# Kernel optimization log

Hardware: AMD Instinct MI355X
Metric: run time of the kernel (lower is better)

The kernel has to match this reference:

```python
import jax, jax.numpy as jnp
import numpy as np

B, C, Q, E = 32, 1024, 128, 512

def setup_inputs() -> dict:
    key = jax.random.key(0)
    k1, k2, k3 = jax.random.split(key, 3)
    context = jax.random.normal(k1, (B, C, E), dtype=jnp.float32)
    question = jax.random.normal(k2, (B, Q, E), dtype=jnp.float32)
    # ws = [ws_q | ws_c | ws_m], matching cat([q, ctx, q*ctx]) order
    ws = jax.random.normal(k3, (3 * E,), dtype=jnp.float32) * (1.0 / np.sqrt(E))
    return {"context": context, "question": question, "ws": ws}

def reference(context, question, ws):
    ws_q, ws_c, ws_m = ws[:E], ws[E:2 * E], ws[2 * E:]
    # similarity[b,c,q] = ws_q.q[b,q] + ws_c.c[b,c] + ws_m.(q[b,q]*c[b,c])
    sim = (jnp.einsum('bqe,e->bq', question, ws_q)[:, None, :]
           + jnp.einsum('bce,e->bc', context, ws_c)[:, :, None]
           + jnp.einsum('bce,bqe,e->bcq', context, question, ws_m))  # (B,C,Q)
    c2q = jnp.einsum('bcq,bqe->bce', jax.nn.softmax(sim, axis=2), question)  # (B,C,E)
    q2c_w = jax.nn.softmax(jnp.max(sim, axis=2), axis=1)  # (B,C)
    q2c = jnp.einsum('bc,bce->be', q2c_w, context)[:, None, :]  # (B,1,E)
    return (c2q, q2c)
```

## Files before the change

kernel.cpp:

```cpp
#include <hip/hip_runtime.h>

#define BB 32
#define CC 1024
#define QQ 128
#define EE 512

typedef unsigned int uint32;
typedef unsigned short u16;
typedef __bf16 bf16x8 __attribute__((ext_vector_type(8)));
typedef float f32x4 __attribute__((ext_vector_type(4)));

#define QMF_OFF  (0u)
#define QTF_OFF  (4u<<20)
#define PV_OFF   (8u<<20)
#define QD_OFF   (12u<<20)
#define MT_OFF   ((12u<<20) + 16384u)
#define ST_OFF   (MT_OFF + 8192u)

__device__ __forceinline__ u16 bfc(float f){
  __bf16 h = (__bf16)f;
  return __builtin_bit_cast(u16, h);
}

__global__ __launch_bounds__(256) void k_prep_qm(const float* __restrict__ q,
                                                 const float* __restrict__ ws,
                                                 unsigned char* __restrict__ wsp){
  const int b = blockIdx.x >> 2, et = blockIdx.x & 3, e0 = et*128;
  __shared__ u16 tile[128*136];
  const int tid = threadIdx.x;
  #pragma unroll
  for (int i=0;i<16;i++){
    int id = tid + i*256;
    int qi = id >> 5;
    int el = (id & 31) << 2;
    float4 v = *(const float4*)(q + (size_t)(b*QQ+qi)*EE + e0 + el);
    float4 m = *(const float4*)(ws + 2*EE + e0 + el);
    float4 c = *(const float4*)(ws +   EE + e0 + el);
    ushort4 u; u.x = bfc(v.x*m.x + c.x); u.y = bfc(v.y*m.y + c.y);
               u.z = bfc(v.z*m.z + c.z); u.w = bfc(v.w*m.w + c.w);
    *(ushort4*)&tile[qi*136 + el] = u;
  }
  __syncthreads();
  const int lane = tid & 63, wv = tid >> 6, l15 = lane & 15, l4 = lane >> 4;
  uint4* qmf = (uint4*)(wsp + QMF_OFF);
  #pragma unroll
  for (int i=0;i<8;i++){
    int f = wv*8 + i;
    int kl = f >> 3, nf = f & 7;
    uint4 u = *(const uint4*)&tile[(nf*16 + l15)*136 + kl*32 + l4*8];
    qmf[(size_t)((b*16 + et*4 + kl)*8 + nf)*64 + lane] = u;
  }
}

__global__ __launch_bounds__(256) void k_prep_qt(const float* __restrict__ q,
                                                 unsigned char* __restrict__ wsp){
  const int b = blockIdx.x >> 2, et = blockIdx.x & 3, e0 = et*128;
  __shared__ u16 tile[128*136];
  const int tid = threadIdx.x;
  #pragma unroll
  for (int i=0;i<16;i++){
    int id = tid + i*256;
    int qi = id >> 5;
    int el = (id & 31) << 2;
    float4 v = *(const float4*)(q + (size_t)(b*QQ+qi)*EE + e0 + el);
    ushort4 u; u.x = bfc(v.x); u.y = bfc(v.y); u.z = bfc(v.z); u.w = bfc(v.w);
    *(ushort4*)&tile[qi*136 + el] = u;
  }
  __syncthreads();
  const int lane = tid & 63, wv = tid >> 6, l15 = lane & 15, l4 = lane >> 4;
  uint4* qtf = (uint4*)(wsp + QTF_OFF);
  #pragma unroll
  for (int i=0;i<8;i++){
    int f = wv*8 + i;
    int ks2 = f >> 3, nl = f & 7, ne = et*8 + nl;
    uint32 x[4];
    #pragma unroll
    for (int p=0;p<4;p++){
      u16 t0 = tile[(ks2*32 + l4*8 + 2*p    )*136 + nl*16 + l15];
      u16 t1 = tile[(ks2*32 + l4*8 + 2*p + 1)*136 + nl*16 + l15];
      x[p] = (uint32)t0 | ((uint32)t1 << 16);
    }
    uint4 u; u.x = x[0]; u.y = x[1]; u.z = x[2]; u.w = x[3];
    qtf[(size_t)((b*4 + ks2)*32 + ne)*64 + lane] = u;
  }
}

__global__ __launch_bounds__(256) void k_prep_qd(const float* __restrict__ q,
                                                 const float* __restrict__ ws,
                                                 unsigned char* __restrict__ wsp){
  const int row = blockIdx.x*4 + (threadIdx.x >> 6);
  const int lane = threadIdx.x & 63;
  const float4* qr = (const float4*)(q + (size_t)row*EE) + lane*2;
  const float4* wq = (const float4*)ws + lane*2;
  float4 v0 = qr[0], v1 = qr[1], a0 = wq[0], a1 = wq[1];
  float dot = v0.x*a0.x + v0.y*a0.y + v0.z*a0.z + v0.w*a0.w
            + v1.x*a1.x + v1.y*a1.y + v1.z*a1.z + v1.w*a1.w;
  #pragma unroll
  for (int off=1; off<64; off<<=1) dot += __shfl_xor(dot, off);
  if (lane == 0) ((float*)(wsp + QD_OFF))[row] = dot;
}

__global__ __launch_bounds__(256, 4) void k_main(const float* __restrict__ ctx,
                                                 unsigned char* __restrict__ wsp,
                                                 float* __restrict__ out){
  __shared__ __align__(16) unsigned char Ast[2][8192];
  __shared__ float smax_s[2][2][16];
  __shared__ float ssum_s[2][2][16];
  __shared__ float wrow_s[2][2][16];

  const int bid = blockIdx.x;
  const int sw  = (bid & 7)*128 + (bid >> 3);
  const int b   = sw >> 5;
  const int t   = sw & 31;
  const int tid = threadIdx.x;
  const int lane = tid & 63;
  const int w    = tid >> 6;
  const int rg   = w >> 1;
  const int h    = w & 1;
  const int l15  = lane & 15;
  const int l4   = lane >> 4;
  const int r0   = t*32 + rg*16;

  const float* qdp = (const float*)(wsp + QD_OFF) + b*QQ + h*64 + l15;
  float qd[4];
  #pragma unroll
  for (int n=0;n<4;n++) qd[n] = qdp[n*16];

  const unsigned char* cbase = (const unsigned char*)(ctx + (size_t)(b*CC + t*32)*EE);
  int srcoff[2];
  #pragma unroll
  for (int j=0;j<2;j++){
    int row = j*16 + w*4 + (lane>>4);
    int gp  = (lane & 15) ^ (row & 7);
    srcoff[j] = row*2048 + gp*16;
  }
  auto stage = [&](int c){
    unsigned char* bufb = Ast[c & 1];
    #pragma unroll
    for (int j=0;j<2;j++){
      const unsigned char* g = cbase + srcoff[j] + c*256;
      __builtin_amdgcn_global_load_lds(
        (const __attribute__((address_space(1))) uint32*)g,
        (__attribute__((address_space(3))) uint32*)(bufb + j*4096 + w*1024),
        16, 0, 0);
    }
  };

  f32x4 acc[4];
  #pragma unroll
  for (int n=0;n<4;n++) acc[n] = (f32x4){0.f,0.f,0.f,0.f};
  const int arow = rg*16 + l15;
  const int a7   = arow & 7;
  const uint4* qmf = (const uint4*)(wsp + QMF_OFF) + (size_t)b*8192 + h*256 + lane;

  stage(0);
  __syncthreads();
  #pragma unroll
  for (int c=0; c<8; c++){
    if (c < 7) stage(c+1);
    const unsigned char* ab = Ast[c&1] + arow*256;
    #pragma unroll
    for (int s=0; s<2; s++){
      uint4 f0 = *(const uint4*)(ab + ((s*8 + ((l4*2+0) ^ a7))*16));
      uint4 f1 = *(const uint4*)(ab + ((s*8 + ((l4*2+1) ^ a7))*16));
      const float* p0 = (const float*)&f0;
      const float* p1 = (const float*)&f1;
      bf16x8 af;
      af[0]=(__bf16)p0[0]; af[1]=(__bf16)p0[1]; af[2]=(__bf16)p0[2]; af[3]=(__bf16)p0[3];
      af[4]=(__bf16)p1[0]; af[5]=(__bf16)p1[1]; af[6]=(__bf16)p1[2]; af[7]=(__bf16)p1[3];
      #pragma unroll
      for (int n=0;n<4;n++){
        bf16x8 bq = __builtin_bit_cast(bf16x8, qmf[((c*2+s)*8 + n)*64]);
        acc[n] = __builtin_amdgcn_mfma_f32_16x16x32_bf16(af, bq, acc[n], 0, 0, 0);
      }
    }
    __syncthreads();
  }

  float mxh[4];
  #pragma unroll
  for (int r=0;r<4;r++){
    float m = -3.0e38f;
    #pragma unroll
    for (int n=0;n<4;n++){
      float v = acc[n][r] + qd[n];
      acc[n][r] = v;
      m = fmaxf(m, v);
    }
    m = fmaxf(m, __shfl_xor(m,1));
    m = fmaxf(m, __shfl_xor(m,2));
    m = fmaxf(m, __shfl_xor(m,4));
    m = fmaxf(m, __shfl_xor(m,8));
    mxh[r] = m;
  }
  if (l15 == 0){
    #pragma unroll
    for (int r=0;r<4;r++) smax_s[rg][h][l4*4 + r] = mxh[r];
  }
  __syncthreads();
  float mx[4];
  #pragma unroll
  for (int r=0;r<4;r++) mx[r] = fmaxf(smax_s[rg][0][l4*4+r], smax_s[rg][1][l4*4+r]);

  u16* pfr = (u16*)Ast[0];
  const int l4p = l15 >> 3;
  const int jj  = l15 & 7;
  #pragma unroll
  for (int r=0;r<4;r++){
    float s = 0.f;
    #pragma unroll
    for (int n=0;n<4;n++){
      float p = __expf(acc[n][r] - mx[r]);
      __bf16 hb = (__bf16)p;
      s += (float)hb;
      pfr[(rg*4 + (h<<1) + (n>>1))*512 + ((((n&1)<<1)|l4p)*16 + l4*4 + r)*8 + jj] = __builtin_bit_cast(u16, hb);
    }
    s += __shfl_xor(s,1); s += __shfl_xor(s,2); s += __shfl_xor(s,4); s += __shfl_xor(s,8);
    if (l15 == 0) ssum_s[rg][h][l4*4 + r] = s;
  }

  float m16 = fmaxf(fmaxf(mx[0],mx[1]), fmaxf(mx[2],mx[3]));
  m16 = fmaxf(m16, __shfl_xor(m16,16));
  m16 = fmaxf(m16, __shfl_xor(m16,32));
  float wr[4], s16 = 0.f;
  #pragma unroll
  for (int r=0;r<4;r++){ wr[r] = __expf(mx[r] - m16); s16 += wr[r]; }
  s16 += __shfl_xor(s16,16);
  s16 += __shfl_xor(s16,32);
  if (l15 == 0){
    #pragma unroll
    for (int r=0;r<4;r++) wrow_s[rg][h][l4*4 + r] = wr[r];
  }
  if (h == 0 && lane == 0){
    ((float*)(wsp + MT_OFF))[b*64 + t*2 + rg] = m16;
    ((float*)(wsp + ST_OFF))[b*64 + t*2 + rg] = s16;
  }
  __syncthreads();
  float rden[4];
  #pragma unroll
  for (int r=0;r<4;r++) rden[r] = 1.f/(ssum_s[rg][0][l4*4+r] + ssum_s[rg][1][l4*4+r]);

  const uint4* qt4 = (const uint4*)(wsp + QTF_OFF) + (size_t)b*8192 + lane;
  const uint4* pf  = (const uint4*)(Ast[0] + rg*4096);
  float* ob = out + (size_t)(b*CC + r0)*EE + h*256;
  #pragma unroll
  for (int pp=0; pp<2; pp++){
    f32x4 acc2[8];
    #pragma unroll
    for (int n2=0;n2<8;n2++) acc2[n2] = (f32x4){0.f,0.f,0.f,0.f};
    #pragma unroll
    for (int ks2=0; ks2<4; ks2++){
      bf16x8 a = __builtin_bit_cast(bf16x8, pf[ks2*64 + lane]);
      #pragma unroll
      for (int n2=0;n2<8;n2++){
        const int ne = h*16 + pp*8 + n2;
        bf16x8 bq = __builtin_bit_cast(bf16x8, qt4[(ks2*32 + ne)*64]);
        acc2[n2] = __builtin_amdgcn_mfma_f32_16x16x32_bf16(a, bq, acc2[n2], 0, 0, 0);
      }
    }
    #pragma unroll
    for (int n2=0;n2<8;n2++){
      #pragma unroll
      for (int r=0;r<4;r++)
        ob[(size_t)(l4*4 + r)*EE + pp*128 + n2*16 + l15] = acc2[n2][r]*rden[r];
    }
  }

  {
    const float4* cb = (const float4*)(ctx + (size_t)(b*CC + r0)*EE + h*256) + lane;
    float4 a4; a4.x = 0.f; a4.y = 0.f; a4.z = 0.f; a4.w = 0.f;
    #pragma unroll
    for (int rr=0; rr<16; rr++){
      float wv = wrow_s[rg][h][rr];
      float4 g = cb[(size_t)rr*128];
      a4.x = fmaf(wv, g.x, a4.x); a4.y = fmaf(wv, g.y, a4.y);
      a4.z = fmaf(wv, g.z, a4.z); a4.w = fmaf(wv, g.w, a4.w);
    }
    float* pv = (float*)(wsp + PV_OFF) + (size_t)(b*64 + t*2 + rg)*EE + h*256 + lane*4;
    *(float4*)pv = a4;
  }
}

__global__ __launch_bounds__(256) void k_fin(unsigned char* __restrict__ wsp,
                                             float* __restrict__ out){
  const int b = blockIdx.x;
  __shared__ float sc_s[64];
  const int tid = threadIdx.x;
  if (tid < 64){
    float Mg = ((const float*)(wsp + MT_OFF))[b*64 + tid];
    float Sg = ((const float*)(wsp + ST_OFF))[b*64 + tid];
    float M = Mg;
    #pragma unroll
    for (int off=1; off<64; off<<=1) M = fmaxf(M, __shfl_xor(M, off));
    float ev = __expf(Mg - M);
    float ds = ev * Sg;
    #pragma unroll
    for (int off=1; off<64; off<<=1) ds += __shfl_xor(ds, off);
    sc_s[tid] = ev / ds;
  }
  __syncthreads();
  const float* pv = (const float*)(wsp + PV_OFF) + (size_t)b*64*EE;
  float a0 = 0.f, a1 = 0.f;
  #pragma unroll 8
  for (int g=0; g<64; g++){
    float s = sc_s[g];
    a0 = fmaf(s, pv[g*EE + tid],       a0);
    a1 = fmaf(s, pv[g*EE + tid + 256], a1);
  }
  size_t base = (size_t)BB*CC*EE + (size_t)b*EE;
  out[base + tid]       = a0;
  out[base + tid + 256] = a1;
}

extern "C" void kernel_launch(void* const* d_in, const int* in_sizes, int n_in,
                              void* d_out, int out_size, void* d_ws, size_t ws_size,
                              hipStream_t stream){
  const float* ctx = (const float*)d_in[0];
  const float* q   = (const float*)d_in[1];
  const float* ws  = (const float*)d_in[2];
  float* out = (float*)d_out;
  unsigned char* wsp = (unsigned char*)d_ws;

  k_prep_qm<<<dim3(BB*4),    dim3(256), 0, stream>>>(q, ws, wsp);
  k_prep_qt<<<dim3(BB*4),    dim3(256), 0, stream>>>(q, wsp);
  k_prep_qd<<<dim3(BB*QQ/4), dim3(256), 0, stream>>>(q, ws, wsp);
  k_main   <<<dim3(1024),    dim3(256), 0, stream>>>(ctx, wsp, out);
  k_fin    <<<dim3(BB),      dim3(256), 0, stream>>>(wsp, out);
}
```

Baseline: 62.64 us.

## Load full context tile to registers, convert to bf16 once, prefetch MFMA operands

Replaces the double-buffered global_load_lds staging of fp32 context chunks with a single bulk register load of the whole 32x512 tile. The tile is converted to bf16 once and stored into a swizzled 32KB LDS buffer, so the per-chunk __syncthreads and the per-MFMA fp32-to-bf16 conversion go away. Both GEMM loops now software-pipeline their B-operand loads one or two steps ahead and preload the P fragments into registers. The cost is more LDS (32KB instead of 16KB) and many more live registers, which may lower occupancy under the 4-blocks launch bound and removes the overlap between context loading and compute.

```diff
diff --git a/kernel.cpp b/kernel.cpp
--- a/kernel.cpp
+++ b/kernel.cpp
@@ -103,7 +103,7 @@
 __global__ __launch_bounds__(256, 4) void k_main(const float* __restrict__ ctx,
                                                  unsigned char* __restrict__ wsp,
                                                  float* __restrict__ out){
-  __shared__ __align__(16) unsigned char Ast[2][8192];
+  __shared__ __align__(16) unsigned char Ast[32*1024];
   __shared__ float smax_s[2][2][16];
   __shared__ float ssum_s[2][2][16];
   __shared__ float wrow_s[2][2][16];
@@ -126,55 +126,61 @@
   #pragma unroll
   for (int n=0;n<4;n++) qd[n] = qdp[n*16];
 
-  const unsigned char* cbase = (const unsigned char*)(ctx + (size_t)(b*CC + t*32)*EE);
-  int srcoff[2];
-  #pragma unroll
-  for (int j=0;j<2;j++){
-    int row = j*16 + w*4 + (lane>>4);
-    int gp  = (lane & 15) ^ (row & 7);
-    srcoff[j] = row*2048 + gp*16;
-  }
-  auto stage = [&](int c){
-    unsigned char* bufb = Ast[c & 1];
-    #pragma unroll
-    for (int j=0;j<2;j++){
-      const unsigned char* g = cbase + srcoff[j] + c*256;
-      __builtin_amdgcn_global_load_lds(
-        (const __attribute__((address_space(1))) uint32*)g,
-        (__attribute__((address_space(3))) uint32*)(bufb + j*4096 + w*1024),
-        16, 0, 0);
-    }
-  };
+  const int srow = w*8 + (lane >> 3);
+  const int scol = (lane & 7)*64;
+  const float4* src = (const float4*)(ctx + (size_t)(b*CC + t*32 + srow)*EE + scol);
+  float4 v[16];
+  #pragma unroll
+  for (int j=0;j<16;j++) v[j] = src[j];
+
+  {
+    unsigned char* drow = Ast + srow*1024;
+    const int dswz = (srow & 7) << 4;
+    #pragma unroll
+    for (int i=0;i<8;i++){
+      float4 x = v[2*i], y = v[2*i+1];
+      uint4 u;
+      u.x = (uint32)bfc(x.x) | ((uint32)bfc(x.y) << 16);
+      u.y = (uint32)bfc(x.z) | ((uint32)bfc(x.w) << 16);
+      u.z = (uint32)bfc(y.x) | ((uint32)bfc(y.y) << 16);
+      u.w = (uint32)bfc(y.z) | ((uint32)bfc(y.w) << 16);
+      *(uint4*)(drow + ((((lane & 7)*128) + i*16) ^ dswz)) = u;
+    }
+  }
+  __syncthreads();
+
+  const int arow = rg*16 + l15;
+  const unsigned char* ap = Ast + arow*1024;
+  const int a7 = (arow & 7) << 4;
+  const uint4* qmf = (const uint4*)(wsp + QMF_OFF) + (size_t)b*8192 + h*256 + lane;
 
   f32x4 acc[4];
   #pragma unroll
   for (int n=0;n<4;n++) acc[n] = (f32x4){0.f,0.f,0.f,0.f};
-  const int arow = rg*16 + l15;
-  const int a7   = arow & 7;
-  const uint4* qmf = (const uint4*)(wsp + QMF_OFF) + (size_t)b*8192 + h*256 + lane;
-
-  stage(0);
-  __syncthreads();
-  #pragma unroll
-  for (int c=0; c<8; c++){
-    if (c < 7) stage(c+1);
-    const unsigned char* ab = Ast[c&1] + arow*256;
-    #pragma unroll
-    for (int s=0; s<2; s++){
-      uint4 f0 = *(const uint4*)(ab + ((s*8 + ((l4*2+0) ^ a7))*16));
-      uint4 f1 = *(const uint4*)(ab + ((s*8 + ((l4*2+1) ^ a7))*16));
-      const float* p0 = (const float*)&f0;
-      const float* p1 = (const float*)&f1;
-      bf16x8 af;
-      af[0]=(__bf16)p0[0]; af[1]=(__bf16)p0[1]; af[2]=(__bf16)p0[2]; af[3]=(__bf16)p0[3];
-      af[4]=(__bf16)p1[0]; af[5]=(__bf16)p1[1]; af[6]=(__bf16)p1[2]; af[7]=(__bf16)p1[3];
+
+  bf16x8 afc = __builtin_bit_cast(bf16x8, *(const uint4*)(ap + ((0*64 + l4*16) ^ a7)));
+  uint4 bq0[4], bq1[4];
+  #pragma unroll
+  for (int n=0;n<4;n++) bq0[n] = qmf[(0*8 + n)*64];
+  #pragma unroll
+  for (int n=0;n<4;n++) bq1[n] = qmf[(1*8 + n)*64];
+
+  #pragma unroll
+  for (int ks=0; ks<16; ks++){
+    bf16x8 afn;
+    if (ks < 15)
+      afn = __builtin_bit_cast(bf16x8, *(const uint4*)(ap + (((ks+1)*64 + l4*16) ^ a7)));
+    uint4 bqn[4];
+    if (ks < 14){
       #pragma unroll
-      for (int n=0;n<4;n++){
-        bf16x8 bq = __builtin_bit_cast(bf16x8, qmf[((c*2+s)*8 + n)*64]);
-        acc[n] = __builtin_amdgcn_mfma_f32_16x16x32_bf16(af, bq, acc[n], 0, 0, 0);
-      }
-    }
-    __syncthreads();
+      for (int n=0;n<4;n++) bqn[n] = qmf[((ks+2)*8 + n)*64];
+    }
+    #pragma unroll
+    for (int n=0;n<4;n++)
+      acc[n] = __builtin_amdgcn_mfma_f32_16x16x32_bf16(afc, __builtin_bit_cast(bf16x8, bq0[n]), acc[n], 0, 0, 0);
+    afc = afn;
+    #pragma unroll
+    for (int n=0;n<4;n++){ bq0[n] = bq1[n]; bq1[n] = bqn[n]; }
   }
 
   float mxh[4];
@@ -183,9 +189,9 @@
     float m = -3.0e38f;
     #pragma unroll
     for (int n=0;n<4;n++){
-      float v = acc[n][r] + qd[n];
-      acc[n][r] = v;
-      m = fmaxf(m, v);
+      float vv = acc[n][r] + qd[n];
+      acc[n][r] = vv;
+      m = fmaxf(m, vv);
     }
     m = fmaxf(m, __shfl_xor(m,1));
     m = fmaxf(m, __shfl_xor(m,2));
@@ -202,7 +208,7 @@
   #pragma unroll
   for (int r=0;r<4;r++) mx[r] = fmaxf(smax_s[rg][0][l4*4+r], smax_s[rg][1][l4*4+r]);
 
-  u16* pfr = (u16*)Ast[0];
+  u16* pfr = (u16*)Ast;
   const int l4p = l15 >> 3;
   const int jj  = l15 & 7;
   #pragma unroll
@@ -241,22 +247,35 @@
   for (int r=0;r<4;r++) rden[r] = 1.f/(ssum_s[rg][0][l4*4+r] + ssum_s[rg][1][l4*4+r]);
 
   const uint4* qt4 = (const uint4*)(wsp + QTF_OFF) + (size_t)b*8192 + lane;
-  const uint4* pf  = (const uint4*)(Ast[0] + rg*4096);
+  const uint4* pf  = (const uint4*)(Ast + rg*4096);
+  bf16x8 pa[4];
+  #pragma unroll
+  for (int ks2=0; ks2<4; ks2++) pa[ks2] = __builtin_bit_cast(bf16x8, pf[ks2*64 + lane]);
   float* ob = out + (size_t)(b*CC + r0)*EE + h*256;
+
   #pragma unroll
   for (int pp=0; pp<2; pp++){
+    const int ne0 = h*16 + pp*8;
     f32x4 acc2[8];
     #pragma unroll
     for (int n2=0;n2<8;n2++) acc2[n2] = (f32x4){0.f,0.f,0.f,0.f};
-    #pragma unroll
-    for (int ks2=0; ks2<4; ks2++){
-      bf16x8 a = __builtin_bit_cast(bf16x8, pf[ks2*64 + lane]);
+    uint4 bqc[4];
+    #pragma unroll
+    for (int n=0;n<4;n++) bqc[n] = qt4[(0*32 + ne0 + n)*64];
+    #pragma unroll
+    for (int u=0; u<8; u++){
+      const int ks2 = u >> 1, hf = u & 1;
+      uint4 bqn[4];
+      if (u < 7){
+        const int u2 = u + 1;
+        #pragma unroll
+        for (int n=0;n<4;n++) bqn[n] = qt4[((u2>>1)*32 + ne0 + (u2&1)*4 + n)*64];
+      }
       #pragma unroll
-      for (int n2=0;n2<8;n2++){
-        const int ne = h*16 + pp*8 + n2;
-        bf16x8 bq = __builtin_bit_cast(bf16x8, qt4[(ks2*32 + ne)*64]);
-        acc2[n2] = __builtin_amdgcn_mfma_f32_16x16x32_bf16(a, bq, acc2[n2], 0, 0, 0);
-      }
+      for (int n=0;n<4;n++)
+        acc2[hf*4+n] = __builtin_amdgcn_mfma_f32_16x16x32_bf16(pa[ks2], __builtin_bit_cast(bf16x8, bqc[n]), acc2[hf*4+n], 0, 0, 0);
+      #pragma unroll
+      for (int n=0;n<4;n++) bqc[n] = bqn[n];
     }
     #pragma unroll
     for (int n2=0;n2<8;n2++){
```

After: 68.37 us. 1.09x slower.

## Restructure main kernel into 64-row, 512-thread blocks with one-shot bf16 context tile

Applied to the files above, without the earlier changes.

Each block now handles 64 context rows with 8 waves instead of 32 rows with 4. The whole context tile is loaded once, converted to bf16 and stored in a swizzled LDS buffer. The question-side fragments are held in registers, and the second GEMM streams Q-transposed tiles through double-buffered LDS with async global-to-LDS loads. The row softmax no longer subtracts the row max before exp: it clamps the logit at 80 and gathers max and sum across waves through shared memory. This removes one reduction pass and a barrier, but can lose accuracy when logits are large.

```diff
diff --git a/kernel.cpp b/kernel.cpp
--- a/kernel.cpp
+++ b/kernel.cpp
@@ -20,6 +20,9 @@
 __device__ __forceinline__ u16 bfc(float f){
   __bf16 h = (__bf16)f;
   return __builtin_bit_cast(u16, h);
+}
+__device__ __forceinline__ float bf2f(uint32 lo16){
+  return __builtin_bit_cast(float, lo16 << 16);
 }
 
 __global__ __launch_bounds__(256) void k_prep_qm(const float* __restrict__ q,
@@ -100,183 +103,190 @@
   if (lane == 0) ((float*)(wsp + QD_OFF))[row] = dot;
 }
 
-__global__ __launch_bounds__(256, 4) void k_main(const float* __restrict__ ctx,
-                                                 unsigned char* __restrict__ wsp,
-                                                 float* __restrict__ out){
-  __shared__ __align__(16) unsigned char Ast[2][8192];
-  __shared__ float smax_s[2][2][16];
-  __shared__ float ssum_s[2][2][16];
-  __shared__ float wrow_s[2][2][16];
+__global__ __attribute__((amdgpu_flat_work_group_size(512, 512)))
+           __attribute__((amdgpu_waves_per_eu(4, 4)))
+void k_main(const float* __restrict__ ctx,
+            unsigned char* __restrict__ wsp,
+            float* __restrict__ out){
+  __shared__ __align__(16) unsigned char tile[65536];
+  __shared__ __align__(16) float mx_s[64*8];
+  __shared__ __align__(16) float sm_s[64*8];
+  __shared__ float wrow_s[4][16];
 
   const int bid = blockIdx.x;
-  const int sw  = (bid & 7)*128 + (bid >> 3);
-  const int b   = sw >> 5;
-  const int t   = sw & 31;
+  const int sw  = (bid & 7)*64 + (bid >> 3);
+  const int b   = sw >> 4;
+  const int t   = sw & 15;
   const int tid = threadIdx.x;
   const int lane = tid & 63;
   const int w    = tid >> 6;
-  const int rg   = w >> 1;
-  const int h    = w & 1;
   const int l15  = lane & 15;
   const int l4   = lane >> 4;
-  const int r0   = t*32 + rg*16;
-
-  const float* qdp = (const float*)(wsp + QD_OFF) + b*QQ + h*64 + l15;
-  float qd[4];
-  #pragma unroll
-  for (int n=0;n<4;n++) qd[n] = qdp[n*16];
-
-  const unsigned char* cbase = (const unsigned char*)(ctx + (size_t)(b*CC + t*32)*EE);
-  int srcoff[2];
-  #pragma unroll
-  for (int j=0;j<2;j++){
-    int row = j*16 + w*4 + (lane>>4);
-    int gp  = (lane & 15) ^ (row & 7);
-    srcoff[j] = row*2048 + gp*16;
-  }
-  auto stage = [&](int c){
-    unsigned char* bufb = Ast[c & 1];
+  const int rg   = w >> 1;
+  const int eh   = w & 1;
+
+  const float4* cb4 = (const float4*)(ctx + (size_t)(b*CC + t*64)*EE);
+  {
+    float4 v[16];
+    #pragma unroll
+    for (int i=0;i<16;i++) v[i] = cb4[i*512 + tid];
+    const int colb = (tid & 127)*8;
+    #pragma unroll
+    for (int i=0;i<16;i++){
+      int row = i*4 + (tid >> 7);
+      uint2 u;
+      u.x = (uint32)bfc(v[i].x) | ((uint32)bfc(v[i].y) << 16);
+      u.y = (uint32)bfc(v[i].z) | ((uint32)bfc(v[i].w) << 16);
+      *(uint2*)(tile + row*1024 + (colb ^ ((row & 7) << 4))) = u;
+    }
+  }
+  const uint4* qmf4 = (const uint4*)(wsp + QMF_OFF);
+  bf16x8 a[16];
+  #pragma unroll
+  for (int ks=0; ks<16; ks++)
+    a[ks] = __builtin_bit_cast(bf16x8, qmf4[(size_t)((b*16 + ks)*8 + w)*64 + lane]);
+  const float4 qdv = *(const float4*)((const float*)(wsp + QD_OFF) + b*QQ + w*16 + l4*4);
+  __syncthreads();
+
+  f32x4 acc[4];
+  #pragma unroll
+  for (int cc=0;cc<4;cc++) acc[cc] = (f32x4){0.f,0.f,0.f,0.f};
+  #pragma unroll
+  for (int ks=0; ks<16; ks++){
+    #pragma unroll
+    for (int cc=0; cc<4; cc++){
+      const int row = cc*16 + l15;
+      bf16x8 bf = __builtin_bit_cast(bf16x8,
+        *(const uint4*)(tile + row*1024 + ((ks*64 + l4*16) ^ ((row & 7) << 4))));
+      acc[cc] = __builtin_amdgcn_mfma_f32_16x16x32_bf16(a[ks], bf, acc[cc], 0, 0, 0);
+    }
+  }
+  __syncthreads();
+
+  {
+    float pm[4], ps[4];
+    #pragma unroll
+    for (int cc=0; cc<4; cc++){
+      float m = -3.0e38f, s = 0.f;
+      u16 hb[4];
+      #pragma unroll
+      for (int r=0;r<4;r++){
+        float vv = acc[cc][r] + qdv[r];
+        vv = fminf(vv, 80.f);
+        m = fmaxf(m, vv);
+        u16 h = bfc(__expf(vv));
+        hb[r] = h;
+        s += bf2f(h);
+      }
+      uint2 u; u.x = (uint32)hb[0] | ((uint32)hb[1]<<16);
+               u.y = (uint32)hb[2] | ((uint32)hb[3]<<16);
+      *(uint2*)(tile + (cc*4 + (w>>1))*1024 + (((w&1)*2 + (l4>>1))*16 + l15)*16 + (l4&1)*8) = u;
+      m = fmaxf(m, __shfl_xor(m, 16)); m = fmaxf(m, __shfl_xor(m, 32));
+      s += __shfl_xor(s, 16);          s += __shfl_xor(s, 32);
+      pm[cc] = m; ps[cc] = s;
+    }
+    if (l4 == 0){
+      #pragma unroll
+      for (int cc=0; cc<4; cc++){
+        mx_s[(cc*16 + l15)*8 + w] = pm[cc];
+        sm_s[(cc*16 + l15)*8 + w] = ps[cc];
+      }
+    }
+  }
+  __syncthreads();
+
+  float rden[4];
+  #pragma unroll
+  for (int r=0;r<4;r++){
+    const int c = rg*16 + l4*4 + r;
+    f32x4 s0 = *(const f32x4*)&sm_s[c*8];
+    f32x4 s1 = *(const f32x4*)&sm_s[c*8 + 4];
+    rden[r] = 1.f/(s0[0]+s0[1]+s0[2]+s0[3]+s1[0]+s1[1]+s1[2]+s1[3]);
+  }
+
+  if (eh == 0){
+    float mf[4];
+    #pragma unroll
+    for (int r=0;r<4;r++){
+      const int c = rg*16 + l4*4 + r;
+      f32x4 m0 = *(const f32x4*)&mx_s[c*8];
+      f32x4 m1 = *(const f32x4*)&mx_s[c*8 + 4];
+      mf[r] = fmaxf(fmaxf(fmaxf(m0[0],m0[1]), fmaxf(m0[2],m0[3])),
+                    fmaxf(fmaxf(m1[0],m1[1]), fmaxf(m1[2],m1[3])));
+    }
+    float m16 = fmaxf(fmaxf(mf[0],mf[1]), fmaxf(mf[2],mf[3]));
+    m16 = fmaxf(m16, __shfl_xor(m16, 16));
+    m16 = fmaxf(m16, __shfl_xor(m16, 32));
+    float wr[4], s16 = 0.f;
+    #pragma unroll
+    for (int r=0;r<4;r++){ wr[r] = __expf(mf[r] - m16); s16 += wr[r]; }
+    s16 += __shfl_xor(s16, 16);
+    s16 += __shfl_xor(s16, 32);
+    if (l15 == 0){
+      #pragma unroll
+      for (int r=0;r<4;r++) wrow_s[rg][l4*4 + r] = wr[r];
+    }
+    if (lane == 0){
+      ((float*)(wsp + MT_OFF))[b*64 + t*4 + rg] = m16;
+      ((float*)(wsp + ST_OFF))[b*64 + t*4 + rg] = s16;
+    }
+  }
+
+  bf16x8 pa[4];
+  #pragma unroll
+  for (int k2=0;k2<4;k2++)
+    pa[k2] = __builtin_bit_cast(bf16x8, *(const uint4*)(tile + (rg*4 + k2)*1024 + lane*16));
+
+  unsigned char* qstage = tile + 16384;
+  const unsigned char* qtfb = wsp + QTF_OFF + (size_t)b*131072;
+  auto dma = [&](int p){
     #pragma unroll
     for (int j=0;j<2;j++){
-      const unsigned char* g = cbase + srcoff[j] + c*256;
+      const int f = w*2 + j;
+      const int ks2 = f >> 2, nl = f & 3;
+      const unsigned char* g = qtfb + (size_t)(ks2*32 + p*4 + nl)*1024 + lane*16;
       __builtin_amdgcn_global_load_lds(
         (const __attribute__((address_space(1))) uint32*)g,
-        (__attribute__((address_space(3))) uint32*)(bufb + j*4096 + w*1024),
+        (__attribute__((address_space(3))) uint32*)(qstage + (p&1)*16384 + f*1024),
         16, 0, 0);
     }
   };
-
-  f32x4 acc[4];
-  #pragma unroll
-  for (int n=0;n<4;n++) acc[n] = (f32x4){0.f,0.f,0.f,0.f};
-  const int arow = rg*16 + l15;
-  const int a7   = arow & 7;
-  const uint4* qmf = (const uint4*)(wsp + QMF_OFF) + (size_t)b*8192 + h*256 + lane;
-
-  stage(0);
-  __syncthreads();
-  #pragma unroll
-  for (int c=0; c<8; c++){
-    if (c < 7) stage(c+1);
-    const unsigned char* ab = Ast[c&1] + arow*256;
-    #pragma unroll
-    for (int s=0; s<2; s++){
-      uint4 f0 = *(const uint4*)(ab + ((s*8 + ((l4*2+0) ^ a7))*16));
-      uint4 f1 = *(const uint4*)(ab + ((s*8 + ((l4*2+1) ^ a7))*16));
-      const float* p0 = (const float*)&f0;
-      const float* p1 = (const float*)&f1;
-      bf16x8 af;
-      af[0]=(__bf16)p0[0]; af[1]=(__bf16)p0[1]; af[2]=(__bf16)p0[2]; af[3]=(__bf16)p0[3];
-      af[4]=(__bf16)p1[0]; af[5]=(__bf16)p1[1]; af[6]=(__bf16)p1[2]; af[7]=(__bf16)p1[3];
-      #pragma unroll
-      for (int n=0;n<4;n++){
-        bf16x8 bq = __builtin_bit_cast(bf16x8, qmf[((c*2+s)*8 + n)*64]);
-        acc[n] = __builtin_amdgcn_mfma_f32_16x16x32_bf16(af, bq, acc[n], 0, 0, 0);
-      }
+  dma(0);
+  __syncthreads();
+
+  float* ob = out + (size_t)(b*CC + t*64 + rg*16)*EE;
+  #pragma unroll
+  for (int p=0; p<8; p++){
+    if (p < 7) dma(p+1);
+    const unsigned char* qs = qstage + (p&1)*16384;
+    f32x4 ac0 = (f32x4){0.f,0.f,0.f,0.f};
+    f32x4 ac1 = (f32x4){0.f,0.f,0.f,0.f};
+    #pragma unroll
+    for (int k2=0;k2<4;k2++){
+      bf16x8 b0 = __builtin_bit_cast(bf16x8, *(const uint4*)(qs + (k2*4 + eh*2 + 0)*1024 + lane*16));
+      bf16x8 b1 = __builtin_bit_cast(bf16x8, *(const uint4*)(qs + (k2*4 + eh*2 + 1)*1024 + lane*16));
+      ac0 = __builtin_amdgcn_mfma_f32_16x16x32_bf16(pa[k2], b0, ac0, 0, 0, 0);
+      ac1 = __builtin_amdgcn_mfma_f32_16x16x32_bf16(pa[k2], b1, ac1, 0, 0, 0);
+    }
+    #pragma unroll
+    for (int r=0;r<4;r++){
+      ob[(size_t)(l4*4 + r)*EE + p*64 + eh*32 +  0 + l15] = ac0[r]*rden[r];
+      ob[(size_t)(l4*4 + r)*EE + p*64 + eh*32 + 16 + l15] = ac1[r]*rden[r];
     }
     __syncthreads();
   }
 
-  float mxh[4];
-  #pragma unroll
-  for (int r=0;r<4;r++){
-    float m = -3.0e38f;
-    #pragma unroll
-    for (int n=0;n<4;n++){
-      float v = acc[n][r] + qd[n];
-      acc[n][r] = v;
-      m = fmaxf(m, v);
-    }
-    m = fmaxf(m, __shfl_xor(m,1));
-    m = fmaxf(m, __shfl_xor(m,2));
-    m = fmaxf(m, __shfl_xor(m,4));
-    m = fmaxf(m, __shfl_xor(m,8));
-    mxh[r] = m;
-  }
-  if (l15 == 0){
-    #pragma unroll
-    for (int r=0;r<4;r++) smax_s[rg][h][l4*4 + r] = mxh[r];
-  }
-  __syncthreads();
-  float mx[4];
-  #pragma unroll
-  for (int r=0;r<4;r++) mx[r] = fmaxf(smax_s[rg][0][l4*4+r], smax_s[rg][1][l4*4+r]);
-
-  u16* pfr = (u16*)Ast[0];
-  const int l4p = l15 >> 3;
-  const int jj  = l15 & 7;
-  #pragma unroll
-  for (int r=0;r<4;r++){
-    float s = 0.f;
-    #pragma unroll
-    for (int n=0;n<4;n++){
-      float p = __expf(acc[n][r] - mx[r]);
-      __bf16 hb = (__bf16)p;
-      s += (float)hb;
-      pfr[(rg*4 + (h<<1) + (n>>1))*512 + ((((n&1)<<1)|l4p)*16 + l4*4 + r)*8 + jj] = __builtin_bit_cast(u16, hb);
-    }
-    s += __shfl_xor(s,1); s += __shfl_xor(s,2); s += __shfl_xor(s,4); s += __shfl_xor(s,8);
-    if (l15 == 0) ssum_s[rg][h][l4*4 + r] = s;
-  }
-
-  float m16 = fmaxf(fmaxf(mx[0],mx[1]), fmaxf(mx[2],mx[3]));
-  m16 = fmaxf(m16, __shfl_xor(m16,16));
-  m16 = fmaxf(m16, __shfl_xor(m16,32));
-  float wr[4], s16 = 0.f;
-  #pragma unroll
-  for (int r=0;r<4;r++){ wr[r] = __expf(mx[r] - m16); s16 += wr[r]; }
-  s16 += __shfl_xor(s16,16);
-  s16 += __shfl_xor(s16,32);
-  if (l15 == 0){
-    #pragma unroll
-    for (int r=0;r<4;r++) wrow_s[rg][h][l4*4 + r] = wr[r];
-  }
-  if (h == 0 && lane == 0){
-    ((float*)(wsp + MT_OFF))[b*64 + t*2 + rg] = m16;
-    ((float*)(wsp + ST_OFF))[b*64 + t*2 + rg] = s16;
-  }
-  __syncthreads();
-  float rden[4];
-  #pragma unroll
-  for (int r=0;r<4;r++) rden[r] = 1.f/(ssum_s[rg][0][l4*4+r] + ssum_s[rg][1][l4*4+r]);
-
-  const uint4* qt4 = (const uint4*)(wsp + QTF_OFF) + (size_t)b*8192 + lane;
-  const uint4* pf  = (const uint4*)(Ast[0] + rg*4096);
-  float* ob = out + (size_t)(b*CC + r0)*EE + h*256;
-  #pragma unroll
-  for (int pp=0; pp<2; pp++){
-    f32x4 acc2[8];
-    #pragma unroll
-    for (int n2=0;n2<8;n2++) acc2[n2] = (f32x4){0.f,0.f,0.f,0.f};
-    #pragma unroll
-    for (int ks2=0; ks2<4; ks2++){
-      bf16x8 a = __builtin_bit_cast(bf16x8, pf[ks2*64 + lane]);
-      #pragma unroll
-      for (int n2=0;n2<8;n2++){
-        const int ne = h*16 + pp*8 + n2;
-        bf16x8 bq = __builtin_bit_cast(bf16x8, qt4[(ks2*32 + ne)*64]);
-        acc2[n2] = __builtin_amdgcn_mfma_f32_16x16x32_bf16(a, bq, acc2[n2], 0, 0, 0);
-      }
-    }
-    #pragma unroll
-    for (int n2=0;n2<8;n2++){
-      #pragma unroll
-      for (int r=0;r<4;r++)
-        ob[(size_t)(l4*4 + r)*EE + pp*128 + n2*16 + l15] = acc2[n2][r]*rden[r];
-    }
-  }
-
   {
-    const float4* cb = (const float4*)(ctx + (size_t)(b*CC + r0)*EE + h*256) + lane;
+    const float4* cq = (const float4*)(ctx + (size_t)(b*CC + t*64 + rg*16)*EE + eh*256) + lane;
     float4 a4; a4.x = 0.f; a4.y = 0.f; a4.z = 0.f; a4.w = 0.f;
     #pragma unroll
     for (int rr=0; rr<16; rr++){
-      float wv = wrow_s[rg][h][rr];
-      float4 g = cb[(size_t)rr*128];
+      float wv = wrow_s[rg][rr];
+      float4 g = cq[(size_t)rr*128];
       a4.x = fmaf(wv, g.x, a4.x); a4.y = fmaf(wv, g.y, a4.y);
       a4.z = fmaf(wv, g.z, a4.z); a4.w = fmaf(wv, g.w, a4.w);
     }
-    float* pv = (float*)(wsp + PV_OFF) + (size_t)(b*64 + t*2 + rg)*EE + h*256 + lane*4;
+    float* pv = (float*)(wsp + PV_OFF) + (size_t)(b*64 + t*4 + rg)*EE + eh*256 + lane*4;
     *(float4*)pv = a4;
   }
 }
@@ -324,6 +334,6 @@
   k_prep_qm<<<dim3(BB*4),    dim3(256), 0, stream>>>(q, ws, wsp);
   k_prep_qt<<<dim3(BB*4),    dim3(256), 0, stream>>>(q, wsp);
   k_prep_qd<<<dim3(BB*QQ/4), dim3(256), 0, stream>>>(q, ws, wsp);
-  k_main   <<<dim3(1024),    dim3(256), 0, stream>>>(ctx, wsp, out);
+  k_main   <<<dim3(512),     dim3(512), 0, stream>>>(ctx, wsp, out);
   k_fin    <<<dim3(BB),      dim3(256), 0, stream>>>(wsp, out);
 }
```

After: 58.58 us. 6.5% less time.
